# Optimization experiments

Measured on AMD Instinct MI355X. Metric: run time of the kernel, lower is better.

## Reference

```python
import jax, jax.numpy as jnp
import numpy as np

B, IN_DIM, OUT_DIM, CB_DIM = 8192, 4096, 4096, 1  # L = OUT_DIM codebooks, 2 codewords each


def setup_inputs() -> dict:
    key = jax.random.key(0)
    k_x, k_w, k_e = jax.random.split(key, 3)
    x = jax.random.normal(k_x, (B, IN_DIM), dtype=jnp.float32)
    W = jax.random.normal(k_w, (IN_DIM, OUT_DIM), dtype=jnp.float32) * (1.0 / np.sqrt(IN_DIM))
    b = jnp.zeros((OUT_DIM,), dtype=jnp.float32)
    # embedding.data.uniform_(-1/2, 1/2)
    embedding = jax.random.uniform(k_e, (OUT_DIM, 2, CB_DIM), dtype=jnp.float32, minval=-0.5, maxval=0.5)
    return {"x": x, "W": W, "b": b, "embedding": embedding}


def reference(x, W, b, embedding):
    L, d = embedding.shape[0], embedding.shape[2]
    # backbone (ToyNet modeled as a single Linear)
    z_e = x @ W + b                                    # [B, L*d]
    z = z_e.reshape(-1, L, d)                          # [B, L, d]
    # squared distance to each of the 2 codewords per codebook
    dist = jnp.sum((z[:, :, None, :] - embedding[None]) ** 2, axis=-1)  # [B, L, 2]
    indices = jnp.argmin(dist, axis=-1)                # [B, L] in {0,1}
    # gather the selected codeword per (batch, codebook)
    quantized = embedding[jnp.arange(L)[None, :], indices]  # [B, L, d]
    quantized = quantized.reshape(-1, L * d)           # [B, L*d]
    # straight-through estimator
    quantized_st = z_e + jax.lax.stop_gradient(quantized - z_e)
    return indices, embedding, quantized_st, z_e
```

## Files before the change

kernel.cpp:

```cpp
#include <hip/hip_runtime.h>

#define B_ROWS  8192
#define IN_DIM  4096
#define OUT_DIM 4096

#define BM 128
#define BN 128
#define BK 16
#define TILES (IN_DIM / BK)
#define PADA 132
#define PADB 132

__global__ __launch_bounds__(256, 2) void vq_fused_gemm(
    const float* __restrict__ X, const float* __restrict__ Wm,
    const float* __restrict__ bvec, const float* __restrict__ emb,
    float* __restrict__ out_idx, float* __restrict__ out_q, float* __restrict__ out_ze)
{
    __shared__ float As[BK * PADA];
    __shared__ float Bs[BK * PADB];

    const int tid  = threadIdx.x;
    const int tx   = tid & 15;
    const int ty   = tid >> 4;
    const int brow = blockIdx.y * BM;
    const int bcol = blockIdx.x * BN;

    const int a_row = tid >> 1;
    const int a_k   = (tid & 1) << 3;
    const int b_k   = tid >> 4;
    const int b_col = (tid & 15) << 3;

    const float* Aptr = X  + (size_t)(brow + a_row) * IN_DIM + a_k;
    const float* Bptr = Wm + (size_t)b_k * OUT_DIM + bcol + b_col;

    float acc_tot[2][2][4][4];
    float acc_blk[2][2][4][4];
    #pragma unroll
    for (int im = 0; im < 2; ++im)
        #pragma unroll
        for (int jm = 0; jm < 2; ++jm)
            #pragma unroll
            for (int i = 0; i < 4; ++i)
                #pragma unroll
                for (int j = 0; j < 4; ++j) {
                    acc_tot[im][jm][i][j] = 0.0f;
                    acc_blk[im][jm][i][j] = 0.0f;
                }

    for (int t = 0; t < TILES; ++t) {
        const int k0 = t * BK;
        float4 av0 = *reinterpret_cast<const float4*>(Aptr + k0);
        float4 av1 = *reinterpret_cast<const float4*>(Aptr + k0 + 4);
        float4 bv0 = *reinterpret_cast<const float4*>(Bptr + (size_t)k0 * OUT_DIM);
        float4 bv1 = *reinterpret_cast<const float4*>(Bptr + (size_t)k0 * OUT_DIM + 4);
        __syncthreads();
        As[(a_k + 0) * PADA + a_row] = av0.x;
        As[(a_k + 1) * PADA + a_row] = av0.y;
        As[(a_k + 2) * PADA + a_row] = av0.z;
        As[(a_k + 3) * PADA + a_row] = av0.w;
        As[(a_k + 4) * PADA + a_row] = av1.x;
        As[(a_k + 5) * PADA + a_row] = av1.y;
        As[(a_k + 6) * PADA + a_row] = av1.z;
        As[(a_k + 7) * PADA + a_row] = av1.w;
        *reinterpret_cast<float4*>(&Bs[b_k * PADB + b_col])     = bv0;
        *reinterpret_cast<float4*>(&Bs[b_k * PADB + b_col + 4]) = bv1;
        __syncthreads();

        #pragma unroll
        for (int kk = 0; kk < BK; ++kk) {
            float4 a0 = *reinterpret_cast<const float4*>(&As[kk * PADA + ty * 4]);
            float4 a1 = *reinterpret_cast<const float4*>(&As[kk * PADA + 64 + ty * 4]);
            float4 b0 = *reinterpret_cast<const float4*>(&Bs[kk * PADB + tx * 4]);
            float4 b1 = *reinterpret_cast<const float4*>(&Bs[kk * PADB + 64 + tx * 4]);
            const float* ap[2] = { (const float*)&a0, (const float*)&a1 };
            const float* bp[2] = { (const float*)&b0, (const float*)&b1 };
            #pragma unroll
            for (int im = 0; im < 2; ++im)
                #pragma unroll
                for (int jm = 0; jm < 2; ++jm)
                    #pragma unroll
                    for (int i = 0; i < 4; ++i)
                        #pragma unroll
                        for (int j = 0; j < 4; ++j)
                            acc_blk[im][jm][i][j] =
                                fmaf(ap[im][i], bp[jm][j], acc_blk[im][jm][i][j]);
        }

        if (((t + 1) & 31) == 0) {
            #pragma unroll
            for (int im = 0; im < 2; ++im)
                #pragma unroll
                for (int jm = 0; jm < 2; ++jm)
                    #pragma unroll
                    for (int i = 0; i < 4; ++i)
                        #pragma unroll
                        for (int j = 0; j < 4; ++j) {
                            acc_tot[im][jm][i][j] += acc_blk[im][jm][i][j];
                            acc_blk[im][jm][i][j] = 0.0f;
                        }
        }
    }

    float e0c[2][4], e1c[2][4], bb[2][4];
    #pragma unroll
    for (int jm = 0; jm < 2; ++jm) {
        const int cb = bcol + jm * 64 + tx * 4;
        #pragma unroll
        for (int j = 0; j < 4; ++j) {
            e0c[jm][j] = emb[2 * (cb + j) + 0];
            e1c[jm][j] = emb[2 * (cb + j) + 1];
            bb[jm][j]  = bvec[cb + j];
        }
    }

    #pragma unroll
    for (int im = 0; im < 2; ++im)
        #pragma unroll
        for (int i = 0; i < 4; ++i) {
            const int r = brow + im * 64 + ty * 4 + i;
            #pragma unroll
            for (int jm = 0; jm < 2; ++jm) {
                float4 vidx, vq, vz;
                float* pi = (float*)&vidx;
                float* pq = (float*)&vq;
                float* pz = (float*)&vz;
                #pragma unroll
                for (int j = 0; j < 4; ++j) {
                    float zb    = acc_tot[im][jm][i][j] + bb[jm][j];
                    float diff0 = zb - e0c[jm][j];
                    float diff1 = zb - e1c[jm][j];
                    float d0    = diff0 * diff0;
                    float d1    = diff1 * diff1;
                    int   idx   = (d1 < d0) ? 1 : 0;
                    float qf    = idx ? e1c[jm][j] : e0c[jm][j];
                    pi[j] = (float)idx;
                    pq[j] = zb + (qf - zb);
                    pz[j] = zb;
                }
                size_t off = (size_t)r * OUT_DIM + bcol + jm * 64 + tx * 4;
                *reinterpret_cast<float4*>(&out_idx[off]) = vidx;
                *reinterpret_cast<float4*>(&out_q[off])   = vq;
                *reinterpret_cast<float4*>(&out_ze[off])  = vz;
            }
        }
}

__global__ void copy_emb(const float* __restrict__ emb, float* __restrict__ out, int n)
{
    int i = blockIdx.x * blockDim.x + threadIdx.x;
    if (i < n) out[i] = emb[i];
}

extern "C" void kernel_launch(void* const* d_in, const int* in_sizes, int n_in,
                              void* d_out, int out_size, void* d_ws, size_t ws_size,
                              hipStream_t stream)
{
    const float* X   = (const float*)d_in[0];
    const float* W   = (const float*)d_in[1];
    const float* b   = (const float*)d_in[2];
    const float* emb = (const float*)d_in[3];

    float* out = (float*)d_out;
    const size_t n_big = (size_t)B_ROWS * OUT_DIM;
    float* out_idx = out;
    float* out_emb = out + n_big;
    float* out_q   = out_emb + (size_t)OUT_DIM * 2;
    float* out_ze  = out_q + n_big;

    dim3 grid(OUT_DIM / BN, B_ROWS / BM);
    vq_fused_gemm<<<grid, dim3(256), 0, stream>>>(X, W, b, emb, out_idx, out_q, out_ze);

    int nemb = OUT_DIM * 2;
    copy_emb<<<(nemb + 255) / 256, 256, 0, stream>>>(emb, out_emb, nemb);
}
```

Before: 3.386 ms.

## Double-buffer shared memory tiles with register prefetch in fused VQ GEMM

Adds two shared-memory buffers for the A and B tiles. The next K-tile's global loads are issued into registers before the current tile's FMA loop and written to the alternate buffer afterwards, so there is one barrier per iteration instead of two. The aim is to hide global load latency behind compute and cut synchronisation. In exchange it doubles LDS use per block and holds the prefetch values in extra live registers, which may put pressure on occupancy under the launch bound of two blocks.

```diff
diff --git a/kernel.cpp b/kernel.cpp
--- a/kernel.cpp
+++ b/kernel.cpp
@@ -16,8 +16,8 @@
     const float* __restrict__ bvec, const float* __restrict__ emb,
     float* __restrict__ out_idx, float* __restrict__ out_q, float* __restrict__ out_ze)
 {
-    __shared__ float As[BK * PADA];
-    __shared__ float Bs[BK * PADB];
+    __shared__ float As[2][BK * PADA];
+    __shared__ float Bs[2][BK * PADB];
 
     const int tid  = threadIdx.x;
     const int tx   = tid & 15;
@@ -47,31 +47,41 @@
                     acc_blk[im][jm][i][j] = 0.0f;
                 }
 
+    {
+        float4 sa0 = *reinterpret_cast<const float4*>(Aptr);
+        float4 sa1 = *reinterpret_cast<const float4*>(Aptr + 4);
+        float4 sb0 = *reinterpret_cast<const float4*>(Bptr);
+        float4 sb1 = *reinterpret_cast<const float4*>(Bptr + 4);
+        As[0][(a_k + 0) * PADA + a_row] = sa0.x;
+        As[0][(a_k + 1) * PADA + a_row] = sa0.y;
+        As[0][(a_k + 2) * PADA + a_row] = sa0.z;
+        As[0][(a_k + 3) * PADA + a_row] = sa0.w;
+        As[0][(a_k + 4) * PADA + a_row] = sa1.x;
+        As[0][(a_k + 5) * PADA + a_row] = sa1.y;
+        As[0][(a_k + 6) * PADA + a_row] = sa1.z;
+        As[0][(a_k + 7) * PADA + a_row] = sa1.w;
+        *reinterpret_cast<float4*>(&Bs[0][b_k * PADB + b_col])     = sb0;
+        *reinterpret_cast<float4*>(&Bs[0][b_k * PADB + b_col + 4]) = sb1;
+    }
+    __syncthreads();
+
     for (int t = 0; t < TILES; ++t) {
-        const int k0 = t * BK;
-        float4 av0 = *reinterpret_cast<const float4*>(Aptr + k0);
-        float4 av1 = *reinterpret_cast<const float4*>(Aptr + k0 + 4);
-        float4 bv0 = *reinterpret_cast<const float4*>(Bptr + (size_t)k0 * OUT_DIM);
-        float4 bv1 = *reinterpret_cast<const float4*>(Bptr + (size_t)k0 * OUT_DIM + 4);
-        __syncthreads();
-        As[(a_k + 0) * PADA + a_row] = av0.x;
-        As[(a_k + 1) * PADA + a_row] = av0.y;
-        As[(a_k + 2) * PADA + a_row] = av0.z;
-        As[(a_k + 3) * PADA + a_row] = av0.w;
-        As[(a_k + 4) * PADA + a_row] = av1.x;
-        As[(a_k + 5) * PADA + a_row] = av1.y;
-        As[(a_k + 6) * PADA + a_row] = av1.z;
-        As[(a_k + 7) * PADA + a_row] = av1.w;
-        *reinterpret_cast<float4*>(&Bs[b_k * PADB + b_col])     = bv0;
-        *reinterpret_cast<float4*>(&Bs[b_k * PADB + b_col + 4]) = bv1;
-        __syncthreads();
+        const int cur = t & 1;
+        float4 ra0, ra1, rb0, rb1;
+        if (t + 1 < TILES) {
+            const int k1 = (t + 1) * BK;
+            ra0 = *reinterpret_cast<const float4*>(Aptr + k1);
+            ra1 = *reinterpret_cast<const float4*>(Aptr + k1 + 4);
+            rb0 = *reinterpret_cast<const float4*>(Bptr + (size_t)k1 * OUT_DIM);
+            rb1 = *reinterpret_cast<const float4*>(Bptr + (size_t)k1 * OUT_DIM + 4);
+        }
 
         #pragma unroll
         for (int kk = 0; kk < BK; ++kk) {
-            float4 a0 = *reinterpret_cast<const float4*>(&As[kk * PADA + ty * 4]);
-            float4 a1 = *reinterpret_cast<const float4*>(&As[kk * PADA + 64 + ty * 4]);
-            float4 b0 = *reinterpret_cast<const float4*>(&Bs[kk * PADB + tx * 4]);
-            float4 b1 = *reinterpret_cast<const float4*>(&Bs[kk * PADB + 64 + tx * 4]);
+            float4 a0 = *reinterpret_cast<const float4*>(&As[cur][kk * PADA + ty * 4]);
+            float4 a1 = *reinterpret_cast<const float4*>(&As[cur][kk * PADA + 64 + ty * 4]);
+            float4 b0 = *reinterpret_cast<const float4*>(&Bs[cur][kk * PADB + tx * 4]);
+            float4 b1 = *reinterpret_cast<const float4*>(&Bs[cur][kk * PADB + 64 + tx * 4]);
             const float* ap[2] = { (const float*)&a0, (const float*)&a1 };
             const float* bp[2] = { (const float*)&b0, (const float*)&b1 };
             #pragma unroll
@@ -98,6 +108,21 @@
                             acc_tot[im][jm][i][j] += acc_blk[im][jm][i][j];
                             acc_blk[im][jm][i][j] = 0.0f;
                         }
+        }
+
+        if (t + 1 < TILES) {
+            const int nxt = cur ^ 1;
+            As[nxt][(a_k + 0) * PADA + a_row] = ra0.x;
+            As[nxt][(a_k + 1) * PADA + a_row] = ra0.y;
+            As[nxt][(a_k + 2) * PADA + a_row] = ra0.z;
+            As[nxt][(a_k + 3) * PADA + a_row] = ra0.w;
+            As[nxt][(a_k + 4) * PADA + a_row] = ra1.x;
+            As[nxt][(a_k + 5) * PADA + a_row] = ra1.y;
+            As[nxt][(a_k + 6) * PADA + a_row] = ra1.z;
+            As[nxt][(a_k + 7) * PADA + a_row] = ra1.w;
+            *reinterpret_cast<float4*>(&Bs[nxt][b_k * PADB + b_col])     = rb0;
+            *reinterpret_cast<float4*>(&Bs[nxt][b_k * PADB + b_col + 4]) = rb1;
+            __syncthreads();
         }
     }
 
```

New measurement: 4.420 ms. 30.5% more time.

## Spill partial-sum accumulator to output buffer to raise occupancy to four blocks

Applied to the files above, without the earlier changes.

Removes the second 64-register accumulator array and instead writes each 512-k partial sum into the out_ze buffer in global memory, read-modify-writing it on later flushes and in the epilogue. The launch bound is raised to request four blocks per SIMD group instead of two, aiming for higher occupancy and better latency hiding. In exchange it adds seven extra global read/write passes over a 128x128 tile per block. A tighter register cap may also force spills of the remaining 64 accumulators.

```diff
diff --git a/kernel.cpp b/kernel.cpp
--- a/kernel.cpp
+++ b/kernel.cpp
@@ -11,7 +11,7 @@
 #define PADA 132
 #define PADB 132
 
-__global__ __launch_bounds__(256, 2) void vq_fused_gemm(
+__global__ __launch_bounds__(256, 4) void vq_fused_gemm(
     const float* __restrict__ X, const float* __restrict__ Wm,
     const float* __restrict__ bvec, const float* __restrict__ emb,
     float* __restrict__ out_idx, float* __restrict__ out_q, float* __restrict__ out_ze)
@@ -33,7 +33,6 @@
     const float* Aptr = X  + (size_t)(brow + a_row) * IN_DIM + a_k;
     const float* Bptr = Wm + (size_t)b_k * OUT_DIM + bcol + b_col;
 
-    float acc_tot[2][2][4][4];
     float acc_blk[2][2][4][4];
     #pragma unroll
     for (int im = 0; im < 2; ++im)
@@ -42,10 +41,8 @@
             #pragma unroll
             for (int i = 0; i < 4; ++i)
                 #pragma unroll
-                for (int j = 0; j < 4; ++j) {
-                    acc_tot[im][jm][i][j] = 0.0f;
+                for (int j = 0; j < 4; ++j)
                     acc_blk[im][jm][i][j] = 0.0f;
-                }
 
     for (int t = 0; t < TILES; ++t) {
         const int k0 = t * BK;
@@ -87,17 +84,42 @@
         }
 
         if (((t + 1) & 31) == 0) {
-            #pragma unroll
-            for (int im = 0; im < 2; ++im)
-                #pragma unroll
-                for (int jm = 0; jm < 2; ++jm)
+            const int f = (t + 1) >> 5;
+            if (f < 8) {
+                #pragma unroll
+                for (int im = 0; im < 2; ++im)
                     #pragma unroll
-                    for (int i = 0; i < 4; ++i)
+                    for (int i = 0; i < 4; ++i) {
+                        const size_t r = (size_t)(brow + im * 64 + ty * 4 + i);
                         #pragma unroll
-                        for (int j = 0; j < 4; ++j) {
-                            acc_tot[im][jm][i][j] += acc_blk[im][jm][i][j];
-                            acc_blk[im][jm][i][j] = 0.0f;
+                        for (int jm = 0; jm < 2; ++jm) {
+                            float* dst = &out_ze[r * OUT_DIM + bcol + jm * 64 + tx * 4];
+                            float4 v;
+                            if (f == 1) {
+                                v.x = acc_blk[im][jm][i][0];
+                                v.y = acc_blk[im][jm][i][1];
+                                v.z = acc_blk[im][jm][i][2];
+                                v.w = acc_blk[im][jm][i][3];
+                            } else {
+                                float4 o = *reinterpret_cast<const float4*>(dst);
+                                v.x = o.x + acc_blk[im][jm][i][0];
+                                v.y = o.y + acc_blk[im][jm][i][1];
+                                v.z = o.z + acc_blk[im][jm][i][2];
+                                v.w = o.w + acc_blk[im][jm][i][3];
+                            }
+                            *reinterpret_cast<float4*>(dst) = v;
                         }
+                    }
+                #pragma unroll
+                for (int im = 0; im < 2; ++im)
+                    #pragma unroll
+                    for (int jm = 0; jm < 2; ++jm)
+                        #pragma unroll
+                        for (int i = 0; i < 4; ++i)
+                            #pragma unroll
+                            for (int j = 0; j < 4; ++j)
+                                acc_blk[im][jm][i][j] = 0.0f;
+            }
         }
     }
 
@@ -117,16 +139,20 @@
     for (int im = 0; im < 2; ++im)
         #pragma unroll
         for (int i = 0; i < 4; ++i) {
-            const int r = brow + im * 64 + ty * 4 + i;
+            const size_t r = (size_t)(brow + im * 64 + ty * 4 + i);
             #pragma unroll
             for (int jm = 0; jm < 2; ++jm) {
+                const size_t off = r * OUT_DIM + bcol + jm * 64 + tx * 4;
+                float4 o = *reinterpret_cast<const float4*>(&out_ze[off]);
                 float4 vidx, vq, vz;
                 float* pi = (float*)&vidx;
                 float* pq = (float*)&vq;
                 float* pz = (float*)&vz;
+                const float* po = (const float*)&o;
                 #pragma unroll
                 for (int j = 0; j < 4; ++j) {
-                    float zb    = acc_tot[im][jm][i][j] + bb[jm][j];
+                    float ztot  = po[j] + acc_blk[im][jm][i][j];
+                    float zb    = ztot + bb[jm][j];
                     float diff0 = zb - e0c[jm][j];
                     float diff1 = zb - e1c[jm][j];
                     float d0    = diff0 * diff0;
@@ -137,7 +163,6 @@
                     pq[j] = zb + (qf - zb);
                     pz[j] = zb;
                 }
-                size_t off = (size_t)r * OUT_DIM + bcol + jm * 64 + tx * 4;
                 *reinterpret_cast<float4*>(&out_idx[off]) = vidx;
                 *reinterpret_cast<float4*>(&out_q[off])   = vq;
                 *reinterpret_cast<float4*>(&out_ze[off])  = vz;
```

Measured after the change: 5.211 ms. +53.9%, slower.
